# Performance work log

Measured on AMD Instinct MI355X. Metric: run time of the kernel, lower is better.

Reference implementation:

```python
import jax, jax.numpy as jnp
import numpy as np

B, S, E = 2, 4096, 512

def setup_inputs() -> dict:
    key = jax.random.key(0)
    kx, kq, kk, kv, ko = jax.random.split(key, 5)
    scale = 1.0 / np.sqrt(E)  # init-style scaling for weights
    return {
        "x": jax.random.normal(kx, (B, S, E), dtype=jnp.float32),
        "Wq": jax.random.normal(kq, (E, E), dtype=jnp.float32) * scale,
        "Wk": jax.random.normal(kk, (E, E), dtype=jnp.float32) * scale,
        "Wv": jax.random.normal(kv, (E, E), dtype=jnp.float32) * scale,
        "Wo": jax.random.normal(ko, (E, E), dtype=jnp.float32) * scale,
        "bo": jnp.zeros((E,), dtype=jnp.float32),
    }

def reference(x, Wq, Wk, Wv, Wo, bo):
    # nn.Linear: y = x @ W.T  (weights stored [out, in])
    q = jnp.einsum("bse,fe->bsf", x, Wq)
    k = jnp.einsum("bse,fe->bsf", x, Wk)
    v = jnp.einsum("bse,fe->bsf", x, Wv)
    inv_scale = 1.0 / jnp.sqrt(jnp.asarray(x.shape[-1], x.dtype))
    scores = jnp.einsum("bqe,bke->bqk", q, k) * inv_scale  # [B,S,S]
    S_len = x.shape[1]
    # torch.triu(ones) keeps j >= i; masked_fill where triu==0 masks j < i
    row = jnp.arange(S_len)[:, None]
    col = jnp.arange(S_len)[None, :]
    keep = col >= row  # [S,S], faithfully anti-causal as in the source
    scores = jnp.where(keep[None, :, :], scores, jnp.asarray(-jnp.inf, scores.dtype))
    attn = jax.nn.softmax(scores, axis=-1)
    # dropout p=0.0 -> identity
    out = jnp.einsum("bqk,bke->bqe", attn, v)
    return jnp.einsum("bse,fe->bsf", out, Wo) + bo
```

## Files before the change

kernel.cpp:

```cpp
#include <hip/hip_runtime.h>
#include <hip/hip_bf16.h>

#define S_LEN 4096
#define E_DIM 512
#define B_DIM 2
#define M_ROWS (B_DIM * S_LEN)

typedef __attribute__((ext_vector_type(8))) short short8;
typedef __attribute__((ext_vector_type(4))) float floatx4;

__device__ __forceinline__ unsigned short f2bf(float f) {
    unsigned u = __float_as_uint(f);
    unsigned r = (u + 0x7fffu + ((u >> 16) & 1u)) >> 16;
    return (unsigned short)r;
}
__device__ __forceinline__ float bf2f(unsigned short u) {
    return __uint_as_float((unsigned)u << 16);
}

__device__ __forceinline__ void async_copy16(unsigned short* lds, const unsigned short* g) {
    auto gp = (const __attribute__((address_space(1))) unsigned int*)g;
    auto lp = (__attribute__((address_space(3))) unsigned int*)lds;
    __builtin_amdgcn_global_load_lds(gp, lp, 16, 0, 0);
}


__global__ __launch_bounds__(256) void convert_bf16(
    const float* __restrict__ x,  const float* __restrict__ wq,
    const float* __restrict__ wk, const float* __restrict__ wv,
    const float* __restrict__ wo, unsigned short* __restrict__ dst)
{
    long i = (long)blockIdx.x * 1024 + (long)threadIdx.x * 4;
    const float* src; long off;
    if      (i < 4194304) { src = x;  off = i; }
    else if (i < 4456448) { src = wq; off = i - 4194304; }
    else if (i < 4718592) { src = wk; off = i - 4456448; }
    else if (i < 4980736) { src = wv; off = i - 4718592; }
    else                  { src = wo; off = i - 4980736; }
    float4 v = *(const float4*)(src + off);
    ushort4 o;
    o.x = f2bf(v.x); o.y = f2bf(v.y); o.z = f2bf(v.z); o.w = f2bf(v.w);
    *(ushort4*)(dst + i) = o;
}

__device__ __forceinline__ void gemm_core(
    const unsigned short* __restrict__ A, const unsigned short* __restrict__ W,
    void* __restrict__ Cv, const float* __restrict__ bias, int mode,
    int m0, int n0)
{
    __shared__ unsigned short As[128 * 32];
    __shared__ unsigned short Bs[128 * 32];
    const int tid = threadIdx.x;
    const int lane = tid & 63, wave = tid >> 6;
    const int wm = wave >> 1, wn = wave & 1;
    const int q4 = lane >> 4, l16 = lane & 15;

    floatx4 acc[4][4];
#pragma unroll
    for (int i = 0; i < 4; ++i)
#pragma unroll
        for (int j = 0; j < 4; ++j) acc[i][j] = (floatx4){0.f, 0.f, 0.f, 0.f};

    const int srow = lane >> 2;
    const int scol = (lane & 3) * 8;

    for (int k0 = 0; k0 < 512; k0 += 32) {
        async_copy16(&As[(wave * 16) * 32],
                     A + (size_t)(m0 + wave * 16 + srow) * 512 + k0 + scol);
        async_copy16(&As[(64 + wave * 16) * 32],
                     A + (size_t)(m0 + 64 + wave * 16 + srow) * 512 + k0 + scol);
        async_copy16(&Bs[(wave * 16) * 32],
                     W + (size_t)(n0 + wave * 16 + srow) * 512 + k0 + scol);
        async_copy16(&Bs[(64 + wave * 16) * 32],
                     W + (size_t)(n0 + 64 + wave * 16 + srow) * 512 + k0 + scol);
        __syncthreads();
        short8 af[4], bfr[4];
#pragma unroll
        for (int i = 0; i < 4; ++i) {
            af[i]  = *(const short8*)&As[(wm * 64 + i * 16 + l16) * 32 + q4 * 8];
            bfr[i] = *(const short8*)&Bs[(wn * 64 + i * 16 + l16) * 32 + q4 * 8];
        }
#pragma unroll
        for (int i = 0; i < 4; ++i)
#pragma unroll
            for (int j = 0; j < 4; ++j)
                acc[i][j] = __builtin_amdgcn_mfma_f32_16x16x32_bf16(af[i], bfr[j], acc[i][j], 0, 0, 0);
        __syncthreads();
    }

    if (mode == 0) {
        unsigned short* C = (unsigned short*)Cv;
#pragma unroll
        for (int i = 0; i < 4; ++i) {
            int rowb = m0 + wm * 64 + i * 16 + q4 * 4;
#pragma unroll
            for (int j = 0; j < 4; ++j) {
                int col = n0 + wn * 64 + j * 16 + l16;
#pragma unroll
                for (int rg = 0; rg < 4; ++rg)
                    C[(size_t)(rowb + rg) * 512 + col] = f2bf(acc[i][j][rg]);
            }
        }
    } else if (mode == 1) {
        unsigned short* C = (unsigned short*)Cv;
#pragma unroll
        for (int i = 0; i < 4; ++i) {
            int grow = m0 + wm * 64 + i * 16 + q4 * 4;
            int b = grow >> 12, s = grow & 4095;
#pragma unroll
            for (int j = 0; j < 4; ++j) {
                int e = n0 + wn * 64 + j * 16 + l16;
                ushort4 pk;
                pk.x = f2bf(acc[i][j][0]); pk.y = f2bf(acc[i][j][1]);
                pk.z = f2bf(acc[i][j][2]); pk.w = f2bf(acc[i][j][3]);
                *(ushort4*)(C + (size_t)b * 512 * 4096 + (size_t)e * 4096 + s) = pk;
            }
        }
    } else {
        float* C = (float*)Cv;
#pragma unroll
        for (int i = 0; i < 4; ++i) {
            int rowb = m0 + wm * 64 + i * 16 + q4 * 4;
#pragma unroll
            for (int j = 0; j < 4; ++j) {
                int col = n0 + wn * 64 + j * 16 + l16;
                float bv = bias[col];
#pragma unroll
                for (int rg = 0; rg < 4; ++rg)
                    C[(size_t)(rowb + rg) * 512 + col] = acc[i][j][rg] + bv;
            }
        }
    }
}

__global__ __launch_bounds__(256) void gemm_qkv(
    const unsigned short* __restrict__ xb,
    const unsigned short* __restrict__ Wqb, const unsigned short* __restrict__ Wkb,
    const unsigned short* __restrict__ Wvb,
    unsigned short* __restrict__ Qb, unsigned short* __restrict__ Kb,
    unsigned short* __restrict__ Vtb)
{
    const int z = blockIdx.z;
    const unsigned short* W = (z == 0) ? Wqb : (z == 1) ? Wkb : Wvb;
    unsigned short* C = (z == 0) ? Qb : (z == 1) ? Kb : Vtb;
    gemm_core(xb, W, C, nullptr, (z == 2) ? 1 : 0, blockIdx.y * 128, blockIdx.x * 128);
}

__global__ __launch_bounds__(256) void gemm_out(
    const unsigned short* __restrict__ AOb, const unsigned short* __restrict__ Wob,
    const float* __restrict__ bo, float* __restrict__ out)
{
    gemm_core(AOb, Wob, out, bo, 2, blockIdx.y * 128, blockIdx.x * 128);
}

__global__ __launch_bounds__(512, 2) void flash_mfma(
    const unsigned short* __restrict__ Qg, const unsigned short* __restrict__ Kg,
    const unsigned short* __restrict__ Vt,
    unsigned short* __restrict__ Oh, float* __restrict__ Lb)
{
    const int bb = blockIdx.y;
    const int ch = blockIdx.z;
    const int tile = blockIdx.x;
    const int i0 = tile * 64;
    const int lo0 = 1024 * ch, hi = 1024 * ch + 1024;
    const int lo = (i0 > lo0) ? i0 : lo0;
    if (lo >= hi) return;

    const int tid = threadIdx.x;
    const int lane = tid & 63, w = tid >> 6;
    const int s = w & 3, h = w >> 2;
    const int q4 = lane >> 4, l16 = lane & 15;
    const float scale = 0.044194173824159216f;
    const float MREF = 4.0f;

    __shared__ float Sred[4][64][36];
    __shared__ unsigned short Plds[64][40];
    __shared__ float Lred[64][8];

    const size_t rowbase = (size_t)bb * S_LEN;
    const size_t vbase   = (size_t)bb * 512 * 4096;

    short8 aq[4][4];
#pragma unroll
    for (int mg = 0; mg < 4; ++mg)
#pragma unroll
        for (int ks = 0; ks < 4; ++ks)
            aq[mg][ks] = *(const short8*)(Qg + (rowbase + i0 + mg * 16 + l16) * 512
                                          + s * 128 + ks * 32 + q4 * 8);

    floatx4 oacc[4][4];
#pragma unroll
    for (int mg = 0; mg < 4; ++mg)
#pragma unroll
        for (int nc = 0; nc < 4; ++nc) oacc[mg][nc] = (floatx4){0.f, 0.f, 0.f, 0.f};

    const int r = tid >> 3;
    const int g = tid & 7;
    float l_acc = 0.f;

    auto step = [&](int j0, short8 (&bkc)[4], short8 (&bkn)[4], int jn) {
        short8 vf[4];
#pragma unroll
        for (int nc = 0; nc < 4; ++nc)
            vf[nc] = *(const short8*)(Vt + vbase
                + (size_t)(w * 64 + nc * 16 + l16) * 4096 + j0 + q4 * 8);
#pragma unroll
        for (int ks = 0; ks < 4; ++ks)
            bkn[ks] = *(const short8*)(Kg + (rowbase + jn + h * 16 + l16) * 512
                                       + s * 128 + ks * 32 + q4 * 8);
        floatx4 sf[4];
#pragma unroll
        for (int mg = 0; mg < 4; ++mg) sf[mg] = (floatx4){0.f, 0.f, 0.f, 0.f};
#pragma unroll
        for (int ks = 0; ks < 4; ++ks)
#pragma unroll
            for (int mg = 0; mg < 4; ++mg)
                sf[mg] = __builtin_amdgcn_mfma_f32_16x16x32_bf16(
                    aq[mg][ks], bkc[ks], sf[mg], 0, 0, 0);
#pragma unroll
        for (int mg = 0; mg < 4; ++mg)
#pragma unroll
            for (int rg = 0; rg < 4; ++rg)
                Sred[s][mg * 16 + q4 * 4 + rg][h * 16 + l16] = sf[mg][rg];
        __syncthreads();

        float4 a0 = *(const float4*)&Sred[0][r][4 * g];
        float4 a1 = *(const float4*)&Sred[1][r][4 * g];
        float4 a2 = *(const float4*)&Sred[2][r][4 * g];
        float4 a3 = *(const float4*)&Sred[3][r][4 * g];
        float sv[4] = { a0.x + a1.x + a2.x + a3.x, a0.y + a1.y + a2.y + a3.y,
                        a0.z + a1.z + a2.z + a3.z, a0.w + a1.w + a2.w + a3.w };
        ushort4 pk;
        float p0, p1, p2, p3;
        {
            int key = j0 + 4 * g;
            int row = i0 + r;
            p0 = (key + 0 >= row) ? __expf(sv[0] * scale - MREF) : 0.f;
            p1 = (key + 1 >= row) ? __expf(sv[1] * scale - MREF) : 0.f;
            p2 = (key + 2 >= row) ? __expf(sv[2] * scale - MREF) : 0.f;
            p3 = (key + 3 >= row) ? __expf(sv[3] * scale - MREF) : 0.f;
        }
        l_acc += p0 + p1 + p2 + p3;
        pk.x = f2bf(p0); pk.y = f2bf(p1); pk.z = f2bf(p2); pk.w = f2bf(p3);
        *(ushort4*)&Plds[r][4 * g] = pk;
        __syncthreads();

        short8 ap[4];
#pragma unroll
        for (int mg = 0; mg < 4; ++mg)
            ap[mg] = *(const short8*)&Plds[mg * 16 + l16][q4 * 8];
#pragma unroll
        for (int mg = 0; mg < 4; ++mg)
#pragma unroll
            for (int nc = 0; nc < 4; ++nc)
                oacc[mg][nc] = __builtin_amdgcn_mfma_f32_16x16x32_bf16(
                    ap[mg], vf[nc], oacc[mg][nc], 0, 0, 0);
    };

    short8 bkA[4], bkB[4];
    int j0 = hi - 32;
#pragma unroll
    for (int ks = 0; ks < 4; ++ks)
        bkA[ks] = *(const short8*)(Kg + (rowbase + j0 + h * 16 + l16) * 512
                                   + s * 128 + ks * 32 + q4 * 8);
    while (j0 >= lo) {
        int jn = (j0 - 32 >= lo) ? j0 - 32 : lo;
        step(j0, bkA, bkB, jn);
        j0 -= 32;
        if (j0 < lo) break;
        jn = (j0 - 32 >= lo) ? j0 - 32 : lo;
        step(j0, bkB, bkA, jn);
        j0 -= 32;
    }
    __syncthreads();

    const int baseArr = (ch == 0) ? 0 : (ch == 1) ? 32 : (ch == 2) ? 96 : 192;
    const int slot = baseArr + bb * 16 * (ch + 1) + tile;

    Lred[r][g] = l_acc;
    __syncthreads();
    if (tid < 64) {
        float sum = 0.f;
#pragma unroll
        for (int gg = 0; gg < 8; ++gg) sum += Lred[tid][gg];
        Lb[(size_t)slot * 64 + tid] = sum;
    }

    unsigned short* Op = Oh + (size_t)slot * 64 * 512;
#pragma unroll
    for (int mg = 0; mg < 4; ++mg)
#pragma unroll
        for (int nc = 0; nc < 4; ++nc)
#pragma unroll
            for (int rg = 0; rg < 4; ++rg)
                Op[(size_t)(mg * 16 + q4 * 4 + rg) * 512 + w * 64 + nc * 16 + l16]
                    = f2bf(oacc[mg][nc][rg]);
}

__global__ __launch_bounds__(256) void flash_merge(
    const unsigned short* __restrict__ Oh, const float* __restrict__ Lb,
    unsigned short* __restrict__ AO)
{
    const int row = blockIdx.x;
    const int c = threadIdx.x * 2;
    const int bb = row >> 12, i = row & 4095;
    const int t = i >> 6, ri = i & 63;
    const int chmin = i >> 10;
    float lsum = 0.f, v0 = 0.f, v1 = 0.f;
#pragma unroll
    for (int ch = 0; ch < 4; ++ch) {
        if (ch < chmin) continue;
        int baseArr = (ch == 0) ? 0 : (ch == 1) ? 32 : (ch == 2) ? 96 : 192;
        int slot = baseArr + bb * 16 * (ch + 1) + t;
        lsum += Lb[(size_t)slot * 64 + ri];
        const unsigned short* p = Oh + (size_t)slot * 64 * 512 + (size_t)ri * 512 + c;
        v0 += bf2f(p[0]);
        v1 += bf2f(p[1]);
    }
    float inv = 1.f / lsum;
    ushort2 o; o.x = f2bf(v0 * inv); o.y = f2bf(v1 * inv);
    *(ushort2*)(AO + (size_t)row * 512 + c) = o;
}

extern "C" void kernel_launch(void* const* d_in, const int* in_sizes, int n_in,
                              void* d_out, int out_size, void* d_ws, size_t ws_size,
                              hipStream_t stream) {
    (void)in_sizes; (void)n_in; (void)out_size; (void)ws_size;
    const float* x  = (const float*)d_in[0];
    const float* Wq = (const float*)d_in[1];
    const float* Wk = (const float*)d_in[2];
    const float* Wv = (const float*)d_in[3];
    const float* Wo = (const float*)d_in[4];
    const float* bo = (const float*)d_in[5];
    float* out = (float*)d_out;

    unsigned short* xb  = (unsigned short*)d_ws;
    unsigned short* Wqb = xb  + 4194304;
    unsigned short* Wkb = Wqb + 262144;
    unsigned short* Wvb = Wkb + 262144;
    unsigned short* Wob = Wvb + 262144;
    unsigned short* Qb  = Wob + 262144;
    unsigned short* Kb  = Qb  + 4194304;
    unsigned short* Vtb = Kb  + 4194304;
    unsigned short* AOb = Vtb + 4194304;
    unsigned short* Ohb = AOb + 4194304;
    float* Lbf = (float*)(Ohb + 10485760);

    convert_bf16<<<5120, 256, 0, stream>>>(x, Wq, Wk, Wv, Wo, xb);

    gemm_qkv<<<dim3(4, 64, 3), 256, 0, stream>>>(xb, Wqb, Wkb, Wvb, Qb, Kb, Vtb);

    flash_mfma<<<dim3(64, 2, 4), 512, 0, stream>>>(Qb, Kb, Vtb, Ohb, Lbf);

    flash_merge<<<8192, 256, 0, stream>>>(Ohb, Lbf, AOb);

    gemm_out<<<dim3(4, 64), 256, 0, stream>>>(AOb, Wob, bo, out);
}
```

Measured before the change: 268.5 us.

## Launch only valid flash tiles via a host-built schedule map, and vectorize score stores

After: 231.7 us. 13.7% less time.

```diff
diff --git a/kernel.cpp b/kernel.cpp
--- a/kernel.cpp
+++ b/kernel.cpp
@@ -24,6 +24,7 @@
     __builtin_amdgcn_global_load_lds(gp, lp, 16, 0, 0);
 }
 
+struct MapArg { unsigned short m[320]; };
 
 __global__ __launch_bounds__(256) void convert_bf16(
     const float* __restrict__ x,  const float* __restrict__ wq,
@@ -156,15 +157,13 @@
 __global__ __launch_bounds__(512, 2) void flash_mfma(
     const unsigned short* __restrict__ Qg, const unsigned short* __restrict__ Kg,
     const unsigned short* __restrict__ Vt,
-    unsigned short* __restrict__ Oh, float* __restrict__ Lb)
-{
-    const int bb = blockIdx.y;
-    const int ch = blockIdx.z;
-    const int tile = blockIdx.x;
+    unsigned short* __restrict__ Oh, float* __restrict__ Lb, MapArg map)
+{
+    const int enc = map.m[blockIdx.x];
+    const int tile = enc & 63, ch = (enc >> 6) & 3, bb = enc >> 8;
     const int i0 = tile * 64;
     const int lo0 = 1024 * ch, hi = 1024 * ch + 1024;
     const int lo = (i0 > lo0) ? i0 : lo0;
-    if (lo >= hi) return;
 
     const int tid = threadIdx.x;
     const int lane = tid & 63, w = tid >> 6;
@@ -216,12 +215,10 @@
 #pragma unroll
             for (int mg = 0; mg < 4; ++mg)
                 sf[mg] = __builtin_amdgcn_mfma_f32_16x16x32_bf16(
-                    aq[mg][ks], bkc[ks], sf[mg], 0, 0, 0);
+                    bkc[ks], aq[mg][ks], sf[mg], 0, 0, 0);
 #pragma unroll
         for (int mg = 0; mg < 4; ++mg)
-#pragma unroll
-            for (int rg = 0; rg < 4; ++rg)
-                Sred[s][mg * 16 + q4 * 4 + rg][h * 16 + l16] = sf[mg][rg];
+            *(floatx4*)&Sred[s][mg * 16 + l16][h * 16 + q4 * 4] = sf[mg];
         __syncthreads();
 
         float4 a0 = *(const float4*)&Sred[0][r][4 * g];
@@ -322,6 +319,34 @@
     *(ushort2*)(AO + (size_t)row * 512 + c) = o;
 }
 
+static MapArg build_map() {
+    int enc[320], steps[320], n = 0;
+    for (int bb = 0; bb < 2; ++bb)
+        for (int ch = 0; ch < 4; ++ch)
+            for (int t = 0; t < 16 * (ch + 1) && t < 64; ++t) {
+                int i0 = t * 64, lo0 = 1024 * ch, hi = lo0 + 1024;
+                int lo = (i0 > lo0) ? i0 : lo0;
+                enc[n] = t | (ch << 6) | (bb << 8);
+                steps[n] = (hi - lo) / 32;
+                ++n;
+            }
+    for (int i = 1; i < n; ++i) {
+        int e = enc[i], st = steps[i], j = i - 1;
+        while (j >= 0 && steps[j] > st) {
+            steps[j + 1] = steps[j]; enc[j + 1] = enc[j]; --j;
+        }
+        steps[j + 1] = st; enc[j + 1] = e;
+    }
+    MapArg mp{};
+    for (int c = 0; c < 64; ++c) {
+        mp.m[c]       = (unsigned short)enc[127 - c];
+        mp.m[256 + c] = (unsigned short)enc[c];
+    }
+    for (int k = 0; k < 192; ++k)
+        mp.m[64 + k] = (unsigned short)enc[128 + k];
+    return mp;
+}
+
 extern "C" void kernel_launch(void* const* d_in, const int* in_sizes, int n_in,
                               void* d_out, int out_size, void* d_ws, size_t ws_size,
                               hipStream_t stream) {
@@ -346,11 +371,13 @@
     unsigned short* Ohb = AOb + 4194304;
     float* Lbf = (float*)(Ohb + 10485760);
 
+    static const MapArg mp = build_map();
+
     convert_bf16<<<5120, 256, 0, stream>>>(x, Wq, Wk, Wv, Wo, xb);
 
     gemm_qkv<<<dim3(4, 64, 3), 256, 0, stream>>>(xb, Wqb, Wkb, Wvb, Qb, Kb, Vtb);
 
-    flash_mfma<<<dim3(64, 2, 4), 512, 0, stream>>>(Qb, Kb, Vtb, Ohb, Lbf);
+    flash_mfma<<<320, 512, 0, stream>>>(Qb, Kb, Vtb, Ohb, Lbf, mp);
 
     flash_merge<<<8192, 256, 0, stream>>>(Ohb, Lbf, AOb);
 
```
